# Kernel optimization log

Measured on AMD Instinct MI355X. Metric: run time of the kernel, lower is better.

Reference implementation:

```python
import jax, jax.numpy as jnp
import numpy as np

EPS = 1e-8

def _gelu(x):
    return jax.nn.gelu(x, approximate=False)  # torch F.gelu default (erf)

def _film_pool(feat, q, film_w, film_b, hid_w, hid_b, fin_w, fin_b):
    # feat: (B,C,H,W), q: (B,Q,E)
    B, C, H, W = feat.shape
    f = feat.reshape(B, C, H * W).transpose(0, 2, 1)            # (B,HW,C)
    gb = q @ film_w + film_b                                    # (B,Q,2C)
    gamma, beta = jnp.split(gb, 2, axis=-1)                     # (B,Q,C) each
    mod = gamma[:, :, None, :] * f[:, None, :, :] + beta[:, :, None, :]  # (B,Q,HW,C)
    h = _gelu(mod @ hid_w + hid_b)                              # (B,Q,HW,Hh)
    attn = jax.nn.sigmoid(h @ fin_w + fin_b)                    # (B,Q,HW,1)
    pooled = (attn * mod).sum(axis=2) / (attn.sum(axis=2) + EPS)  # (B,Q,C)
    return pooled, attn[..., 0]                                 # attn map (B,Q,HW)

def setup_inputs() -> dict:
    key = jax.random.key(0)
    ks = jax.random.split(key, 32)
    B, Q, E, Hh = 2, 32, 768, 128
    chans = [64, 128, 256]
    hws = [(80, 80), (40, 40), (20, 20)]
    d = {}
    d['feat0'] = jax.random.normal(ks[0], (B, chans[0], *hws[0]), jnp.float32)
    d['feat1'] = jax.random.normal(ks[1], (B, chans[1], *hws[1]), jnp.float32)
    d['feat2'] = jax.random.normal(ks[2], (B, chans[2], *hws[2]), jnp.float32)
    d['fact_embeddings'] = jax.random.normal(ks[3], (B, Q, E), jnp.float32)
    for i, C in enumerate(chans):
        d[f'film_w{i}'] = jax.random.normal(ks[4 + 4 * i], (E, 2 * C), jnp.float32) * 0.02
        d[f'film_b{i}'] = jnp.zeros((2 * C,), jnp.float32)
        d[f'hid_w{i}'] = jax.random.normal(ks[5 + 4 * i], (C, Hh), jnp.float32) * 0.05
        d[f'hid_b{i}'] = jnp.zeros((Hh,), jnp.float32)
        d[f'fin_w{i}'] = jax.random.normal(ks[6 + 4 * i], (Hh, 1), jnp.float32) * 0.05
        d[f'fin_b{i}'] = jnp.zeros((1,), jnp.float32)
    in_dim = sum(chans) + hws[-1][0] * hws[-1][1]  # 448 + 400 = 848
    d['mlp_w1'] = jax.random.normal(ks[20], (in_dim, 512), jnp.float32) * 0.02
    d['mlp_b1'] = jnp.zeros((512,), jnp.float32)
    d['mlp_w2'] = jax.random.normal(ks[21], (512, 256), jnp.float32) * 0.02
    d['mlp_b2'] = jnp.zeros((256,), jnp.float32)
    d['mlp_w3'] = jax.random.normal(ks[22], (256, 1), jnp.float32) * 0.02
    d['mlp_b3'] = jnp.zeros((1,), jnp.float32)
    return d

def reference(feat0, feat1, feat2, fact_embeddings,
              film_w0, film_b0, hid_w0, hid_b0, fin_w0, fin_b0,
              film_w1, film_b1, hid_w1, hid_b1, fin_w1, fin_b1,
              film_w2, film_b2, hid_w2, hid_b2, fin_w2, fin_b2,
              mlp_w1, mlp_b1, mlp_w2, mlp_b2, mlp_w3, mlp_b3):
    q = fact_embeddings
    p0, _ = _film_pool(feat0, q, film_w0, film_b0, hid_w0, hid_b0, fin_w0, fin_b0)
    p1, _ = _film_pool(feat1, q, film_w1, film_b1, hid_w1, hid_b1, fin_w1, fin_b1)
    p2, a2 = _film_pool(feat2, q, film_w2, film_b2, hid_w2, hid_b2, fin_w2, fin_b2)
    cat = jnp.concatenate([p0, p1, p2, a2], axis=2)  # (B,Q,848)
    x = _gelu(cat @ mlp_w1 + mlp_b1)
    x = _gelu(x @ mlp_w2 + mlp_b2)
    logits = (x @ mlp_w3 + mlp_b3)[..., 0]  # (B,Q)
    return logits
```

## Files before the change

kernel.cpp:

```cpp
#include <hip/hip_runtime.h>
#include <math.h>

#define BQ 64
#define HH 128
#define EPS 1e-8f

typedef short bf16x8 __attribute__((ext_vector_type(8)));
typedef float f32x4  __attribute__((ext_vector_type(4)));

typedef const __attribute__((address_space(1))) void* gptr_t;
typedef __attribute__((address_space(3))) void* lptr_t;

__device__ __forceinline__ float gelu_exact(float x) {
    return 0.5f * x * (1.0f + erff(x * 0.70710678118654752440f));
}

__device__ __forceinline__ unsigned bf16_rne(float x) {
    unsigned u = __float_as_uint(x);
    return (u + 0x7FFFu + ((u >> 16) & 1u)) >> 16;
}
__device__ __forceinline__ uint2 split_pack(float a, float b) {
    unsigned ha = bf16_rne(a);
    float fa = __uint_as_float(ha << 16);
    unsigned la = bf16_rne(a - fa);
    unsigned hb = bf16_rne(b);
    float fb = __uint_as_float(hb << 16);
    unsigned lb = bf16_rne(b - fb);
    uint2 r; r.x = ha | (hb << 16); r.y = la | (lb << 16);
    return r;
}

__device__ __forceinline__
void pack_feat_body(int i,
                    const float* __restrict__ f0, const float* __restrict__ f1,
                    const float* __restrict__ f2,
                    unsigned short* __restrict__ p0h, unsigned short* __restrict__ p0l,
                    unsigned short* __restrict__ p1h, unsigned short* __restrict__ p1l,
                    unsigned short* __restrict__ p2h, unsigned short* __restrict__ p2l)
{
    const float* f; unsigned short *oh, *ol; int HW; int idx;
    if (i < 102400)      { f = f0; oh = p0h; ol = p0l; HW = 6400; idx = i; }
    else if (i < 153600) { f = f1; oh = p1h; ol = p1l; HW = 1600; idx = i - 102400; }
    else if (i < 179200) { f = f2; oh = p2h; ol = p2l; HW = 400;  idx = i - 153600; }
    else return;
    const int px = idx % HW;
    const int cgb = idx / HW;
    const float* src = f + ((size_t)cgb * 8) * HW + px;
    float a[8];
    #pragma unroll
    for (int k = 0; k < 8; ++k) a[k] = src[(size_t)k * HW];
    unsigned hwd[4], lwd[4];
    #pragma unroll
    for (int k = 0; k < 4; ++k) {
        uint2 p = split_pack(a[2 * k], a[2 * k + 1]);
        hwd[k] = p.x; lwd[k] = p.y;
    }
    *(uint4*)&oh[(size_t)idx * 8] = make_uint4(hwd[0], hwd[1], hwd[2], hwd[3]);
    *(uint4*)&ol[(size_t)idx * 8] = make_uint4(lwd[0], lwd[1], lwd[2], lwd[3]);
}

__global__ __launch_bounds__(256)
void prep1_kernel(const float* __restrict__ f0, const float* __restrict__ f1,
                  const float* __restrict__ f2,
                  unsigned short* __restrict__ p0h, unsigned short* __restrict__ p0l,
                  unsigned short* __restrict__ p1h, unsigned short* __restrict__ p1l,
                  unsigned short* __restrict__ p2h, unsigned short* __restrict__ p2l,
                  const float* __restrict__ qe,
                  const float* __restrict__ fw0, const float* __restrict__ fb0,
                  const float* __restrict__ fw1, const float* __restrict__ fb1,
                  const float* __restrict__ fw2, const float* __restrict__ fb2,
                  float* __restrict__ gb0, float* __restrict__ gb1, float* __restrict__ gb2)
{
    const int tid = threadIdx.x;
    if (blockIdx.x < 700) {
        pack_feat_body(blockIdx.x * 256 + tid, f0, f1, f2, p0h, p0l, p1h, p1l, p2h, p2l);
        return;
    }
    __shared__ float sq[768];
    __shared__ float sP[256];
    const int bb = blockIdx.x - 700;
    const int chunk = bb >> 6, bq = bb & 63;
    int s, o0;
    if (chunk == 0)      { s = 0; o0 = 0; }
    else if (chunk <= 2) { s = 1; o0 = (chunk - 1) * 128; }
    else                 { s = 2; o0 = (chunk - 3) * 128; }
    const float* fw  = s == 0 ? fw0 : s == 1 ? fw1 : fw2;
    const float* fbv = s == 0 ? fb0 : s == 1 ? fb1 : fb2;
    float* gb        = s == 0 ? gb0 : s == 1 ? gb1 : gb2;
    const int twoC = 128 << s;

    for (int i = tid; i < 768; i += 256) sq[i] = qe[bq * 768 + i];
    __syncthreads();
    const int o = o0 + (tid & 127), half = tid >> 7;
    const int e0 = half * 384;
    float a0 = 0.f, a1 = 0.f;
    #pragma unroll 2
    for (int e = 0; e < 384; e += 2) {
        a0 = fmaf(sq[e0 + e],     fw[(e0 + e) * twoC + o],     a0);
        a1 = fmaf(sq[e0 + e + 1], fw[(e0 + e + 1) * twoC + o], a1);
    }
    sP[tid] = a0 + a1;
    __syncthreads();
    if (tid < 128) {
        int oo = o0 + tid;
        gb[bq * twoC + oo] = sP[tid] + sP[tid + 128] + fbv[oo];
    }
}

__global__ __launch_bounds__(256)
void prep2_kernel(const float* __restrict__ gb0, const float* __restrict__ gb1,
                  const float* __restrict__ gb2,
                  const float* __restrict__ hw0_, const float* __restrict__ hb0,
                  const float* __restrict__ hw1_, const float* __restrict__ hb1,
                  const float* __restrict__ hw2_, const float* __restrict__ hb2,
                  unsigned short* __restrict__ g0h, unsigned short* __restrict__ g0l,
                  unsigned short* __restrict__ g1h, unsigned short* __restrict__ g1l,
                  unsigned short* __restrict__ g2h, unsigned short* __restrict__ g2l,
                  float* __restrict__ b20, float* __restrict__ b21, float* __restrict__ b22)
{
    const int tid = threadIdx.x;
    if (blockIdx.x < 1792) {
        int i = blockIdx.x * 256 + tid;
        const float *gb, *hw; unsigned short *oh, *ol; int C, idx;
        if (i < 65536)       { gb = gb0; hw = hw0_; oh = g0h; ol = g0l; C = 64;  idx = i; }
        else if (i < 196608) { gb = gb1; hw = hw1_; oh = g1h; ol = g1l; C = 128; idx = i - 65536; }
        else                 { gb = gb2; hw = hw2_; oh = g2h; ol = g2l; C = 256; idx = i - 196608; }
        const int j  = idx & 127;
        const int cg = (idx >> 7) % (C / 8);
        const int bq = idx / (128 * (C / 8));
        const int c0 = cg * 8;
        const float* g = gb + bq * 2 * C;
        float a[8];
        #pragma unroll
        for (int k = 0; k < 8; ++k) a[k] = g[c0 + k] * hw[(size_t)(c0 + k) * HH + j];
        unsigned hwd[4], lwd[4];
        #pragma unroll
        for (int k = 0; k < 4; ++k) {
            uint2 p = split_pack(a[2 * k], a[2 * k + 1]);
            hwd[k] = p.x; lwd[k] = p.y;
        }
        *(uint4*)&oh[(size_t)idx * 8] = make_uint4(hwd[0], hwd[1], hwd[2], hwd[3]);
        *(uint4*)&ol[(size_t)idx * 8] = make_uint4(lwd[0], lwd[1], lwd[2], lwd[3]);
        return;
    }
    __shared__ float sBeta[256];
    __shared__ float sP[256];
    const int bb = blockIdx.x - 1792;
    const int s = bb >> 6, bq = bb & 63;
    const float* gb = s == 0 ? gb0 : s == 1 ? gb1 : gb2;
    const float* hw = s == 0 ? hw0_ : s == 1 ? hw1_ : hw2_;
    const float* hb = s == 0 ? hb0 : s == 1 ? hb1 : hb2;
    float* b2       = s == 0 ? b20 : s == 1 ? b21 : b22;
    const int C = 64 << s;

    for (int i = tid; i < C; i += 256) sBeta[i] = gb[bq * 2 * C + C + i];
    __syncthreads();
    const int j = tid & 127, half = tid >> 7;
    const int c0 = half * (C / 2);
    float acc = 0.f;
    for (int c = 0; c < C / 2; ++c)
        acc = fmaf(sBeta[c0 + c], hw[(c0 + c) * HH + j], acc);
    sP[tid] = acc;
    __syncthreads();
    if (tid < 128) b2[bq * HH + tid] = hb[tid] + sP[tid] + sP[tid + 128];
}

#define MFMA3(ACC, ALO, AHI, BH, BL)                                            \
    ACC = __builtin_amdgcn_mfma_f32_16x16x32_bf16(ALO, BH, ACC, 0, 0, 0);       \
    ACC = __builtin_amdgcn_mfma_f32_16x16x32_bf16(AHI, BL, ACC, 0, 0, 0);       \
    ACC = __builtin_amdgcn_mfma_f32_16x16x32_bf16(AHI, BH, ACC, 0, 0, 0);

template<int C, bool WRITE_ATTN>
__device__ __forceinline__
void pool_body(const float* __restrict__ feat, int HW,
               const unsigned short* __restrict__ fh, const unsigned short* __restrict__ fl,
               const unsigned short* __restrict__ gwh, const unsigned short* __restrict__ gwl,
               const float* __restrict__ b2, const float* __restrict__ finw,
               const float* __restrict__ finb,
               float* __restrict__ Sout, float* __restrict__ attn_out,
               int b, int qp, int tile,
               unsigned short* sB, float* sAttn)
{
    const int tid  = threadIdx.x;
    const int w    = tid >> 6;
    const int lane = tid & 63;
    const int l15  = lane & 15, l4 = lane >> 4;
    const int px0  = tile * 256;
    constexpr int CG  = C / 8;
    constexpr int NKS = CG / 4;
    const int bq0 = b * 32 + qp * 2;
    const int bq1 = bq0 + 1;
    const float* fbase = feat + (size_t)b * C * HW;

    f32x4 accA[2][8], accB[2][8];
    #pragma unroll
    for (int jt = 0; jt < 8; ++jt) {
        float bv0 = b2[bq0 * HH + jt * 16 + l15];
        float bv1 = b2[bq1 * HH + jt * 16 + l15];
        accA[0][jt] = (f32x4){bv0, bv0, bv0, bv0};
        accA[1][jt] = (f32x4){bv0, bv0, bv0, bv0};
        accB[0][jt] = (f32x4){bv1, bv1, bv1, bv1};
        accB[1][jt] = (f32x4){bv1, bv1, bv1, bv1};
    }

    const int apx0 = min(px0 + (w * 2 + 0) * 16 + l15, HW - 1);
    const int apx1 = min(px0 + (w * 2 + 1) * 16 + l15, HW - 1);
    const unsigned short* fhp = fh + (size_t)b * CG * HW * 8;
    const unsigned short* flp = fl + (size_t)b * CG * HW * 8;
    const unsigned short* qsrc0 = gwh + (size_t)bq0 * CG * 1024;
    const unsigned short* qsrc1 = gwl + (size_t)bq0 * CG * 1024;
    const unsigned short* qsrc2 = gwh + (size_t)bq1 * CG * 1024;
    const unsigned short* qsrc3 = gwl + (size_t)bq1 * CG * 1024;

    const int lane8 = lane * 8;
    const int woff  = __builtin_amdgcn_readfirstlane(w * 512);

    #define STAGE(KS, BUF)                                                       \
    {                                                                            \
        const unsigned short* s0 = qsrc0 + (size_t)(KS) * 4096 + woff + lane8;   \
        const unsigned short* s1 = qsrc1 + (size_t)(KS) * 4096 + woff + lane8;   \
        const unsigned short* s2 = qsrc2 + (size_t)(KS) * 4096 + woff + lane8;   \
        const unsigned short* s3 = qsrc3 + (size_t)(KS) * 4096 + woff + lane8;   \
        __builtin_amdgcn_global_load_lds((gptr_t)s0, (lptr_t)((BUF) + 0    + woff), 16, 0, 0); \
        __builtin_amdgcn_global_load_lds((gptr_t)s1, (lptr_t)((BUF) + 4096 + woff), 16, 0, 0); \
        __builtin_amdgcn_global_load_lds((gptr_t)s2, (lptr_t)((BUF) + 8192 + woff), 16, 0, 0); \
        __builtin_amdgcn_global_load_lds((gptr_t)s3, (lptr_t)((BUF) + 12288 + woff), 16, 0, 0); \
    }

    STAGE(0, sB)

    for (int ks = 0; ks < NKS; ++ks) {
        __syncthreads();
        unsigned short* cur = sB + (ks & 1) * 16384;
        if (ks + 1 < NKS) STAGE(ks + 1, sB + (((ks + 1) & 1) * 16384))

        const size_t arow = (size_t)(ks * 4 + l4) * HW;
        const bf16x8 Ahi0 = *(const bf16x8*)(fhp + (arow + apx0) * 8);
        const bf16x8 Alo0 = *(const bf16x8*)(flp + (arow + apx0) * 8);
        const bf16x8 Ahi1 = *(const bf16x8*)(fhp + (arow + apx1) * 8);
        const bf16x8 Alo1 = *(const bf16x8*)(flp + (arow + apx1) * 8);

        const int bofs = (l4 * 128 + l15) * 8;
        #pragma unroll
        for (int jt = 0; jt < 8; ++jt) {
            const bf16x8 B0h = *(const bf16x8*)(cur + bofs + jt * 128);
            const bf16x8 B0l = *(const bf16x8*)(cur + 4096 + bofs + jt * 128);
            MFMA3(accA[0][jt], Alo0, Ahi0, B0h, B0l)
            MFMA3(accA[1][jt], Alo1, Ahi1, B0h, B0l)
            const bf16x8 B1h = *(const bf16x8*)(cur + 8192 + bofs + jt * 128);
            const bf16x8 B1l = *(const bf16x8*)(cur + 12288 + bofs + jt * 128);
            MFMA3(accB[0][jt], Alo0, Ahi0, B1h, B1l)
            MFMA3(accB[1][jt], Alo1, Ahi1, B1h, B1l)
        }
    }
    #undef STAGE

    const float fb0 = finb[0];
    #pragma unroll
    for (int pt = 0; pt < 2; ++pt) {
        float p0[4] = {0.f, 0.f, 0.f, 0.f};
        float p1[4] = {0.f, 0.f, 0.f, 0.f};
        #pragma unroll
        for (int jt = 0; jt < 8; ++jt) {
            float fwv = finw[jt * 16 + l15];
            #pragma unroll
            for (int r = 0; r < 4; ++r) {
                p0[r] = fmaf(gelu_exact(accA[pt][jt][r]), fwv, p0[r]);
                p1[r] = fmaf(gelu_exact(accB[pt][jt][r]), fwv, p1[r]);
            }
        }
        #pragma unroll
        for (int r = 0; r < 4; ++r) {
            p0[r] += __shfl_xor(p0[r], 1);  p1[r] += __shfl_xor(p1[r], 1);
            p0[r] += __shfl_xor(p0[r], 2);  p1[r] += __shfl_xor(p1[r], 2);
            p0[r] += __shfl_xor(p0[r], 4);  p1[r] += __shfl_xor(p1[r], 4);
            p0[r] += __shfl_xor(p0[r], 8);  p1[r] += __shfl_xor(p1[r], 8);
        }
        if (l15 == 0) {
            #pragma unroll
            for (int r = 0; r < 4; ++r) {
                int lpx = (w * 2 + pt) * 16 + l4 * 4 + r;
                int px  = px0 + lpx;
                float a0v = (px < HW) ? 1.0f / (1.0f + expf(-(p0[r] + fb0))) : 0.0f;
                float a1v = (px < HW) ? 1.0f / (1.0f + expf(-(p1[r] + fb0))) : 0.0f;
                sAttn[lpx]       = a0v;
                sAttn[256 + lpx] = a1v;
                if (WRITE_ATTN && px < HW) {
                    attn_out[bq0 * HW + px] = a0v;
                    attn_out[bq1 * HW + px] = a1v;
                }
            }
        }
    }
    __syncthreads();

    {
        float sa = sAttn[tid];
        #pragma unroll
        for (int d = 1; d < 64; d <<= 1) sa += __shfl_xor(sa, d);
        if (lane == 0) {
            int bqx = (tid < 256) ? bq0 : bq1;
            atomicAdd(&Sout[bqx * (C + 1) + C], sa);
        }
    }

    constexpr int CPW = C / 8;
    #pragma unroll 1
    for (int ci = 0; ci < CPW; ++ci) {
        const int c2 = w * CPW + ci;
        const float* fr = fbase + (size_t)c2 * HW;
        float s0 = 0.f, s1 = 0.f;
        #pragma unroll
        for (int k = 0; k < 4; ++k) {
            int lpx = lane + 64 * k;
            int gc = min(px0 + lpx, HW - 1);
            float fv = fr[gc];
            s0 = fmaf(fv, sAttn[lpx], s0);
            s1 = fmaf(fv, sAttn[256 + lpx], s1);
        }
        #pragma unroll
        for (int d = 1; d < 64; d <<= 1) {
            s0 += __shfl_xor(s0, d);
            s1 += __shfl_xor(s1, d);
        }
        if (lane == 0) {
            atomicAdd(&Sout[bq0 * (C + 1) + c2], s0);
            atomicAdd(&Sout[bq1 * (C + 1) + c2], s1);
        }
    }
}

__global__ __launch_bounds__(512)
void pool_fused(const unsigned short* __restrict__ f0h, const unsigned short* __restrict__ f0l,
                const unsigned short* __restrict__ f1h, const unsigned short* __restrict__ f1l,
                const unsigned short* __restrict__ f2h, const unsigned short* __restrict__ f2l,
                const unsigned short* __restrict__ g0h, const unsigned short* __restrict__ g0l,
                const unsigned short* __restrict__ g1h, const unsigned short* __restrict__ g1l,
                const unsigned short* __restrict__ g2h, const unsigned short* __restrict__ g2l,
                const float* __restrict__ feat0, const float* __restrict__ feat1,
                const float* __restrict__ feat2,
                const float* __restrict__ b20, const float* __restrict__ b21,
                const float* __restrict__ b22,
                const float* __restrict__ finw0, const float* __restrict__ finb0,
                const float* __restrict__ finw1, const float* __restrict__ finb1,
                const float* __restrict__ finw2, const float* __restrict__ finb2,
                float* __restrict__ S0, float* __restrict__ S1, float* __restrict__ S2,
                float* __restrict__ attn2)
{
    __shared__ __align__(16) unsigned short sB[32768];
    float* sAttn = (float*)sB;

    const int blk0 = blockIdx.x;
    const int xcd = blk0 & 7, s = blk0 >> 3;
    int k, t;
    if (s < 8)       { k = s >> 1;            t = s & 1; }
    else if (s < 36) { k = 4 + (s - 8) / 7;   t = (s - 8) % 7; }
    else             { k = 8 + (s - 36) / 25; t = (s - 36) % 25; }
    const int b  = xcd >> 2;
    const int qp = (k & 3) * 4 + (xcd & 3);
    const int sidx = k >> 2;

    if (sidx == 0) {
        pool_body<256, true>(feat2, 400, f2h, f2l, g2h, g2l, b22, finw2, finb2,
                             S2, attn2, b, qp, t, sB, sAttn);
    } else if (sidx == 1) {
        pool_body<128, false>(feat1, 1600, f1h, f1l, g1h, g1l, b21, finw1, finb1,
                              S1, nullptr, b, qp, t, sB, sAttn);
    } else {
        pool_body<64, false>(feat0, 6400, f0h, f0l, g0h, g0l, b20, finw0, finb0,
                             S0, nullptr, b, qp, t, sB, sAttn);
    }
}

__global__ __launch_bounds__(256)
void mlp1_kernel(const float* __restrict__ S0, const float* __restrict__ S1,
                 const float* __restrict__ S2,
                 const float* __restrict__ gb0, const float* __restrict__ gb1,
                 const float* __restrict__ gb2,
                 const float* __restrict__ attn2,
                 const float* __restrict__ w1, const float* __restrict__ b1,
                 float* __restrict__ X1)
{
    __shared__ float sCat[848];
    __shared__ float sP[256];
    const int tid = threadIdx.x, bq = blockIdx.x;

    for (int i = tid; i < 448; i += 256) {
        int sc, c;
        if (i < 64)       { sc = 0; c = i; }
        else if (i < 192) { sc = 1; c = i - 64; }
        else              { sc = 2; c = i - 192; }
        const int C = 64 << sc;
        const float* So = (sc == 0) ? S0 : (sc == 1) ? S1 : S2;
        const float* g  = (sc == 0) ? gb0 : (sc == 1) ? gb1 : gb2;
        float Sa = So[bq * (C + 1) + C];
        float Sf = So[bq * (C + 1) + c];
        float gamma = g[bq * 2 * C + c];
        float beta  = g[bq * 2 * C + C + c];
        sCat[i] = (gamma * Sf + beta * Sa) / (Sa + EPS);
    }
    for (int i = tid; i < 400; i += 256) sCat[448 + i] = attn2[bq * 400 + i];
    __syncthreads();

    const int o = blockIdx.y * 128 + (tid & 127), half = tid >> 7;
    const int k0 = half * 424;
    float a0 = 0.f, a1 = 0.f;
    #pragma unroll 2
    for (int k = 0; k < 424; k += 2) {
        a0 = fmaf(sCat[k0 + k],     w1[(k0 + k) * 512 + o],     a0);
        a1 = fmaf(sCat[k0 + k + 1], w1[(k0 + k + 1) * 512 + o], a1);
    }
    sP[tid] = a0 + a1;
    __syncthreads();
    if (tid < 128) {
        int oo = blockIdx.y * 128 + tid;
        X1[bq * 512 + oo] = sP[tid] + sP[tid + 128] + b1[oo];
    }
}

__global__ __launch_bounds__(256)
void mlp23_kernel(const float* __restrict__ X1,
                  const float* __restrict__ w2, const float* __restrict__ b2,
                  const float* __restrict__ w3, const float* __restrict__ b3,
                  float* __restrict__ out)
{
    __shared__ float sX1[512];
    __shared__ float sX2[256];
    __shared__ float sR[4];
    const int tid = threadIdx.x, bq = blockIdx.x;
    for (int i = tid; i < 512; i += 256) sX1[i] = gelu_exact(X1[bq * 512 + i]);
    __syncthreads();
    float a0 = b2[tid], a1 = 0.f, a2 = 0.f, a3 = 0.f;
    #pragma unroll 4
    for (int k = 0; k < 512; k += 4) {
        a0 = fmaf(sX1[k],     w2[(k)     * 256 + tid], a0);
        a1 = fmaf(sX1[k + 1], w2[(k + 1) * 256 + tid], a1);
        a2 = fmaf(sX1[k + 2], w2[(k + 2) * 256 + tid], a2);
        a3 = fmaf(sX1[k + 3], w2[(k + 3) * 256 + tid], a3);
    }
    sX2[tid] = gelu_exact((a0 + a1) + (a2 + a3));
    __syncthreads();
    float p = sX2[tid] * w3[tid];
    #pragma unroll
    for (int d = 1; d < 64; d <<= 1) p += __shfl_xor(p, d);
    if ((tid & 63) == 0) sR[tid >> 6] = p;
    __syncthreads();
    if (tid == 0) out[bq] = sR[0] + sR[1] + sR[2] + sR[3] + b3[0];
}

extern "C" void kernel_launch(void* const* d_in, const int* in_sizes, int n_in,
                              void* d_out, int out_size, void* d_ws, size_t ws_size,
                              hipStream_t stream)
{
    const float* feat0 = (const float*)d_in[0];
    const float* feat1 = (const float*)d_in[1];
    const float* feat2 = (const float*)d_in[2];
    const float* qe    = (const float*)d_in[3];
    const float* film_w0 = (const float*)d_in[4];
    const float* film_b0 = (const float*)d_in[5];
    const float* hid_w0  = (const float*)d_in[6];
    const float* hid_b0  = (const float*)d_in[7];
    const float* fin_w0  = (const float*)d_in[8];
    const float* fin_b0  = (const float*)d_in[9];
    const float* film_w1 = (const float*)d_in[10];
    const float* film_b1 = (const float*)d_in[11];
    const float* hid_w1  = (const float*)d_in[12];
    const float* hid_b1  = (const float*)d_in[13];
    const float* fin_w1  = (const float*)d_in[14];
    const float* fin_b1  = (const float*)d_in[15];
    const float* film_w2 = (const float*)d_in[16];
    const float* film_b2 = (const float*)d_in[17];
    const float* hid_w2  = (const float*)d_in[18];
    const float* hid_b2  = (const float*)d_in[19];
    const float* fin_w2  = (const float*)d_in[20];
    const float* fin_b2  = (const float*)d_in[21];
    const float* mlp_w1  = (const float*)d_in[22];
    const float* mlp_b1  = (const float*)d_in[23];
    const float* mlp_w2  = (const float*)d_in[24];
    const float* mlp_b2  = (const float*)d_in[25];
    const float* mlp_w3  = (const float*)d_in[26];
    const float* mlp_b3  = (const float*)d_in[27];

    float* ws = (float*)d_ws;
    float* S0    = ws;
    float* S1    = ws + 4160;
    float* S2    = ws + 12416;
    float* gb0   = ws + 28864;
    float* gb1   = ws + 37056;
    float* gb2   = ws + 53440;
    float* b20   = ws + 86208;
    float* b21   = ws + 94400;
    float* b22   = ws + 102592;
    float* attn2 = ws + 110784;
    float* X1    = ws + 136384;

    unsigned short* us = (unsigned short*)(ws + 169216);
    unsigned short* f0h = us;
    unsigned short* f0l = f0h + 819200;
    unsigned short* f1h = f0l + 819200;
    unsigned short* f1l = f1h + 409600;
    unsigned short* f2h = f1l + 409600;
    unsigned short* f2l = f2h + 204800;
    unsigned short* g0h = f2l + 204800;
    unsigned short* g0l = g0h + 524288;
    unsigned short* g1h = g0l + 524288;
    unsigned short* g1l = g1h + 1048576;
    unsigned short* g2h = g1l + 1048576;
    unsigned short* g2l = g2h + 2097152;

    hipMemsetAsync(d_ws, 0, 28864 * sizeof(float), stream);

    prep1_kernel<<<1148, 256, 0, stream>>>(
        feat0, feat1, feat2, f0h, f0l, f1h, f1l, f2h, f2l,
        qe, film_w0, film_b0, film_w1, film_b1, film_w2, film_b2,
        gb0, gb1, gb2);

    prep2_kernel<<<1984, 256, 0, stream>>>(
        gb0, gb1, gb2,
        hid_w0, hid_b0, hid_w1, hid_b1, hid_w2, hid_b2,
        g0h, g0l, g1h, g1l, g2h, g2l,
        b20, b21, b22);

    pool_fused<<<1088, 512, 0, stream>>>(
        f0h, f0l, f1h, f1l, f2h, f2l,
        g0h, g0l, g1h, g1l, g2h, g2l,
        feat0, feat1, feat2,
        b20, b21, b22,
        fin_w0, fin_b0, fin_w1, fin_b1, fin_w2, fin_b2,
        S0, S1, S2, attn2);

    mlp1_kernel<<<dim3(BQ, 4), 256, 0, stream>>>(
        S0, S1, S2, gb0, gb1, gb2, attn2, mlp_w1, mlp_b1, X1);

    mlp23_kernel<<<BQ, 256, 0, stream>>>(
        X1, mlp_w2, mlp_b2, mlp_w3, mlp_b3, (float*)d_out);
}
```

Baseline: 246.7 us.

## Fold memset into prep, pipeline A loads, reorder pool blocks, fuse MLP kernels

The workspace memset moves into extra blocks of prep1, which removes a separate launch. The pool main loop is unrolled by two so the A-fragment global loads for the next K-step are issued before the current MFMAs. The pooled-feature reduction reads the split-bf16 packed features instead of the original fp32 maps, and the block index mapping drops its XCD-aware ordering in favour of a simple linear one. The two MLP kernels become one 512-thread kernel per query, which removes a launch and the X1 round trip, but runs the first layer on only 64 blocks.

After: 268.2 us. +8.7%, slower.

```diff
diff --git a/kernel.cpp b/kernel.cpp
--- a/kernel.cpp
+++ b/kernel.cpp
@@ -28,6 +28,9 @@
     unsigned lb = bf16_rne(b - fb);
     uint2 r; r.x = ha | (hb << 16); r.y = la | (lb << 16);
     return r;
+}
+__device__ __forceinline__ float bf_to_f(unsigned short u) {
+    return __uint_as_float((unsigned)u << 16);
 }
 
 __device__ __forceinline__
@@ -69,11 +72,17 @@
                   const float* __restrict__ fw0, const float* __restrict__ fb0,
                   const float* __restrict__ fw1, const float* __restrict__ fb1,
                   const float* __restrict__ fw2, const float* __restrict__ fb2,
-                  float* __restrict__ gb0, float* __restrict__ gb1, float* __restrict__ gb2)
+                  float* __restrict__ gb0, float* __restrict__ gb1, float* __restrict__ gb2,
+                  float* __restrict__ zws)
 {
     const int tid = threadIdx.x;
     if (blockIdx.x < 700) {
         pack_feat_body(blockIdx.x * 256 + tid, f0, f1, f2, p0h, p0l, p1h, p1l, p2h, p2l);
+        return;
+    }
+    if (blockIdx.x >= 1148) {
+        int idx = (blockIdx.x - 1148) * 256 + tid;
+        if (idx < 28864) zws[idx] = 0.0f;
         return;
     }
     __shared__ float sq[768];
@@ -172,7 +181,7 @@
 
 template<int C, bool WRITE_ATTN>
 __device__ __forceinline__
-void pool_body(const float* __restrict__ feat, int HW,
+void pool_body(int HW,
                const unsigned short* __restrict__ fh, const unsigned short* __restrict__ fl,
                const unsigned short* __restrict__ gwh, const unsigned short* __restrict__ gwl,
                const float* __restrict__ b2, const float* __restrict__ finw,
@@ -190,7 +199,6 @@
     constexpr int NKS = CG / 4;
     const int bq0 = b * 32 + qp * 2;
     const int bq1 = bq0 + 1;
-    const float* fbase = feat + (size_t)b * C * HW;
 
     f32x4 accA[2][8], accB[2][8];
     #pragma unroll
@@ -221,39 +229,57 @@
         const unsigned short* s1 = qsrc1 + (size_t)(KS) * 4096 + woff + lane8;   \
         const unsigned short* s2 = qsrc2 + (size_t)(KS) * 4096 + woff + lane8;   \
         const unsigned short* s3 = qsrc3 + (size_t)(KS) * 4096 + woff + lane8;   \
-        __builtin_amdgcn_global_load_lds((gptr_t)s0, (lptr_t)((BUF) + 0    + woff), 16, 0, 0); \
-        __builtin_amdgcn_global_load_lds((gptr_t)s1, (lptr_t)((BUF) + 4096 + woff), 16, 0, 0); \
-        __builtin_amdgcn_global_load_lds((gptr_t)s2, (lptr_t)((BUF) + 8192 + woff), 16, 0, 0); \
+        __builtin_amdgcn_global_load_lds((gptr_t)s0, (lptr_t)((BUF) + 0     + woff), 16, 0, 0); \
+        __builtin_amdgcn_global_load_lds((gptr_t)s1, (lptr_t)((BUF) + 4096  + woff), 16, 0, 0); \
+        __builtin_amdgcn_global_load_lds((gptr_t)s2, (lptr_t)((BUF) + 8192  + woff), 16, 0, 0); \
         __builtin_amdgcn_global_load_lds((gptr_t)s3, (lptr_t)((BUF) + 12288 + woff), 16, 0, 0); \
     }
 
+    #define LOADA(KS, H0, L0, H1, L1)                                            \
+    {                                                                            \
+        const size_t ar = (size_t)((KS) * 4 + l4) * HW;                          \
+        H0 = *(const bf16x8*)(fhp + (ar + apx0) * 8);                            \
+        L0 = *(const bf16x8*)(flp + (ar + apx0) * 8);                            \
+        H1 = *(const bf16x8*)(fhp + (ar + apx1) * 8);                            \
+        L1 = *(const bf16x8*)(flp + (ar + apx1) * 8);                            \
+    }
+
+    #define MFMAB(CUR, H0, L0, H1, L1)                                           \
+    {                                                                            \
+        const int bofs = (l4 * 128 + l15) * 8;                                   \
+        _Pragma("unroll")                                                        \
+        for (int jt = 0; jt < 8; ++jt) {                                         \
+            const bf16x8 B0h = *(const bf16x8*)((CUR) + bofs + jt * 128);        \
+            const bf16x8 B0l = *(const bf16x8*)((CUR) + 4096 + bofs + jt * 128); \
+            MFMA3(accA[0][jt], L0, H0, B0h, B0l)                                 \
+            MFMA3(accA[1][jt], L1, H1, B0h, B0l)                                 \
+            const bf16x8 B1h = *(const bf16x8*)((CUR) + 8192 + bofs + jt * 128); \
+            const bf16x8 B1l = *(const bf16x8*)((CUR) + 12288 + bofs + jt * 128);\
+            MFMA3(accB[0][jt], L0, H0, B1h, B1l)                                 \
+            MFMA3(accB[1][jt], L1, H1, B1h, B1l)                                 \
+        }                                                                        \
+    }
+
+    bf16x8 cA0h, cA0l, cA1h, cA1l, nA0h, nA0l, nA1h, nA1l;
     STAGE(0, sB)
-
-    for (int ks = 0; ks < NKS; ++ks) {
+    LOADA(0, cA0h, cA0l, cA1h, cA1l)
+
+    #pragma unroll 1
+    for (int ks = 0; ks < NKS; ks += 2) {
         __syncthreads();
-        unsigned short* cur = sB + (ks & 1) * 16384;
-        if (ks + 1 < NKS) STAGE(ks + 1, sB + (((ks + 1) & 1) * 16384))
-
-        const size_t arow = (size_t)(ks * 4 + l4) * HW;
-        const bf16x8 Ahi0 = *(const bf16x8*)(fhp + (arow + apx0) * 8);
-        const bf16x8 Alo0 = *(const bf16x8*)(flp + (arow + apx0) * 8);
-        const bf16x8 Ahi1 = *(const bf16x8*)(fhp + (arow + apx1) * 8);
-        const bf16x8 Alo1 = *(const bf16x8*)(flp + (arow + apx1) * 8);
-
-        const int bofs = (l4 * 128 + l15) * 8;
-        #pragma unroll
-        for (int jt = 0; jt < 8; ++jt) {
-            const bf16x8 B0h = *(const bf16x8*)(cur + bofs + jt * 128);
-            const bf16x8 B0l = *(const bf16x8*)(cur + 4096 + bofs + jt * 128);
-            MFMA3(accA[0][jt], Alo0, Ahi0, B0h, B0l)
-            MFMA3(accA[1][jt], Alo1, Ahi1, B0h, B0l)
-            const bf16x8 B1h = *(const bf16x8*)(cur + 8192 + bofs + jt * 128);
-            const bf16x8 B1l = *(const bf16x8*)(cur + 12288 + bofs + jt * 128);
-            MFMA3(accB[0][jt], Alo0, Ahi0, B1h, B1l)
-            MFMA3(accB[1][jt], Alo1, Ahi1, B1h, B1l)
-        }
+        LOADA(ks + 1, nA0h, nA0l, nA1h, nA1l)
+        STAGE(ks + 1, sB + 16384)
+        MFMAB(sB, cA0h, cA0l, cA1h, cA1l)
+        __syncthreads();
+        if (ks + 2 < NKS) {
+            LOADA(ks + 2, cA0h, cA0l, cA1h, cA1l)
+            STAGE(ks + 2, sB)
+        }
+        MFMAB(sB + 16384, nA0h, nA0l, nA1h, nA1l)
     }
     #undef STAGE
+    #undef LOADA
+    #undef MFMAB
 
     const float fb0 = finb[0];
     #pragma unroll
@@ -308,13 +334,14 @@
     #pragma unroll 1
     for (int ci = 0; ci < CPW; ++ci) {
         const int c2 = w * CPW + ci;
-        const float* fr = fbase + (size_t)c2 * HW;
+        const unsigned short* ph = fhp + ((size_t)(c2 >> 3) * HW) * 8 + (c2 & 7);
+        const unsigned short* pl = flp + ((size_t)(c2 >> 3) * HW) * 8 + (c2 & 7);
         float s0 = 0.f, s1 = 0.f;
         #pragma unroll
         for (int k = 0; k < 4; ++k) {
             int lpx = lane + 64 * k;
             int gc = min(px0 + lpx, HW - 1);
-            float fv = fr[gc];
+            float fv = bf_to_f(ph[(size_t)gc * 8]) + bf_to_f(pl[(size_t)gc * 8]);
             s0 = fmaf(fv, sAttn[lpx], s0);
             s1 = fmaf(fv, sAttn[256 + lpx], s1);
         }
@@ -337,8 +364,6 @@
                 const unsigned short* __restrict__ g0h, const unsigned short* __restrict__ g0l,
                 const unsigned short* __restrict__ g1h, const unsigned short* __restrict__ g1l,
                 const unsigned short* __restrict__ g2h, const unsigned short* __restrict__ g2l,
-                const float* __restrict__ feat0, const float* __restrict__ feat1,
-                const float* __restrict__ feat2,
                 const float* __restrict__ b20, const float* __restrict__ b21,
                 const float* __restrict__ b22,
                 const float* __restrict__ finw0, const float* __restrict__ finb0,
@@ -350,46 +375,48 @@
     __shared__ __align__(16) unsigned short sB[32768];
     float* sAttn = (float*)sB;
 
-    const int blk0 = blockIdx.x;
-    const int xcd = blk0 & 7, s = blk0 >> 3;
-    int k, t;
-    if (s < 8)       { k = s >> 1;            t = s & 1; }
-    else if (s < 36) { k = 4 + (s - 8) / 7;   t = (s - 8) % 7; }
-    else             { k = 8 + (s - 36) / 25; t = (s - 36) % 25; }
-    const int b  = xcd >> 2;
-    const int qp = (k & 3) * 4 + (xcd & 3);
-    const int sidx = k >> 2;
-
-    if (sidx == 0) {
-        pool_body<256, true>(feat2, 400, f2h, f2l, g2h, g2l, b22, finw2, finb2,
+    const int blk = blockIdx.x;
+    if (blk < 64) {
+        int bt = blk >> 4, qp = blk & 15;
+        int b = bt >> 1, t = bt & 1;
+        pool_body<256, true>(400, f2h, f2l, g2h, g2l, b22, finw2, finb2,
                              S2, attn2, b, qp, t, sB, sAttn);
-    } else if (sidx == 1) {
-        pool_body<128, false>(feat1, 1600, f1h, f1l, g1h, g1l, b21, finw1, finb1,
+    } else if (blk < 288) {
+        int bb = blk - 64; int bt = bb >> 4, qp = bb & 15;
+        int b = bt / 7, t = bt % 7;
+        pool_body<128, false>(1600, f1h, f1l, g1h, g1l, b21, finw1, finb1,
                               S1, nullptr, b, qp, t, sB, sAttn);
     } else {
-        pool_body<64, false>(feat0, 6400, f0h, f0l, g0h, g0l, b20, finw0, finb0,
+        int bb = blk - 288; int bt = bb >> 4, qp = bb & 15;
+        int b = bt / 25, t = bt % 25;
+        pool_body<64, false>(6400, f0h, f0l, g0h, g0l, b20, finw0, finb0,
                              S0, nullptr, b, qp, t, sB, sAttn);
     }
 }
 
-__global__ __launch_bounds__(256)
-void mlp1_kernel(const float* __restrict__ S0, const float* __restrict__ S1,
-                 const float* __restrict__ S2,
-                 const float* __restrict__ gb0, const float* __restrict__ gb1,
-                 const float* __restrict__ gb2,
-                 const float* __restrict__ attn2,
-                 const float* __restrict__ w1, const float* __restrict__ b1,
-                 float* __restrict__ X1)
+__global__ __launch_bounds__(512)
+void mlp_fused(const float* __restrict__ S0, const float* __restrict__ S1,
+               const float* __restrict__ S2,
+               const float* __restrict__ gb0, const float* __restrict__ gb1,
+               const float* __restrict__ gb2,
+               const float* __restrict__ attn2,
+               const float* __restrict__ w1, const float* __restrict__ b1,
+               const float* __restrict__ w2, const float* __restrict__ mb2,
+               const float* __restrict__ w3, const float* __restrict__ b3,
+               float* __restrict__ out)
 {
     __shared__ float sCat[848];
-    __shared__ float sP[256];
+    __shared__ float sX1[512];
+    __shared__ float sP[512];
+    __shared__ float sX2[256];
+    __shared__ float sR[4];
     const int tid = threadIdx.x, bq = blockIdx.x;
 
-    for (int i = tid; i < 448; i += 256) {
+    if (tid < 448) {
         int sc, c;
-        if (i < 64)       { sc = 0; c = i; }
-        else if (i < 192) { sc = 1; c = i - 64; }
-        else              { sc = 2; c = i - 192; }
+        if (tid < 64)       { sc = 0; c = tid; }
+        else if (tid < 192) { sc = 1; c = tid - 64; }
+        else                { sc = 2; c = tid - 192; }
         const int C = 64 << sc;
         const float* So = (sc == 0) ? S0 : (sc == 1) ? S1 : S2;
         const float* g  = (sc == 0) ? gb0 : (sc == 1) ? gb1 : gb2;
@@ -397,53 +424,43 @@
         float Sf = So[bq * (C + 1) + c];
         float gamma = g[bq * 2 * C + c];
         float beta  = g[bq * 2 * C + C + c];
-        sCat[i] = (gamma * Sf + beta * Sa) / (Sa + EPS);
-    }
-    for (int i = tid; i < 400; i += 256) sCat[448 + i] = attn2[bq * 400 + i];
-    __syncthreads();
-
-    const int o = blockIdx.y * 128 + (tid & 127), half = tid >> 7;
-    const int k0 = half * 424;
-    float a0 = 0.f, a1 = 0.f;
-    #pragma unroll 2
-    for (int k = 0; k < 424; k += 2) {
-        a0 = fmaf(sCat[k0 + k],     w1[(k0 + k) * 512 + o],     a0);
-        a1 = fmaf(sCat[k0 + k + 1], w1[(k0 + k + 1) * 512 + o], a1);
-    }
-    sP[tid] = a0 + a1;
-    __syncthreads();
-    if (tid < 128) {
-        int oo = blockIdx.y * 128 + tid;
-        X1[bq * 512 + oo] = sP[tid] + sP[tid + 128] + b1[oo];
-    }
-}
-
-__global__ __launch_bounds__(256)
-void mlp23_kernel(const float* __restrict__ X1,
-                  const float* __restrict__ w2, const float* __restrict__ b2,
-                  const float* __restrict__ w3, const float* __restrict__ b3,
-                  float* __restrict__ out)
-{
-    __shared__ float sX1[512];
-    __shared__ float sX2[256];
-    __shared__ float sR[4];
-    const int tid = threadIdx.x, bq = blockIdx.x;
-    for (int i = tid; i < 512; i += 256) sX1[i] = gelu_exact(X1[bq * 512 + i]);
-    __syncthreads();
-    float a0 = b2[tid], a1 = 0.f, a2 = 0.f, a3 = 0.f;
-    #pragma unroll 4
-    for (int k = 0; k < 512; k += 4) {
-        a0 = fmaf(sX1[k],     w2[(k)     * 256 + tid], a0);
-        a1 = fmaf(sX1[k + 1], w2[(k + 1) * 256 + tid], a1);
-        a2 = fmaf(sX1[k + 2], w2[(k + 2) * 256 + tid], a2);
-        a3 = fmaf(sX1[k + 3], w2[(k + 3) * 256 + tid], a3);
-    }
-    sX2[tid] = gelu_exact((a0 + a1) + (a2 + a3));
-    __syncthreads();
-    float p = sX2[tid] * w3[tid];
-    #pragma unroll
-    for (int d = 1; d < 64; d <<= 1) p += __shfl_xor(p, d);
-    if ((tid & 63) == 0) sR[tid >> 6] = p;
+        sCat[tid] = (gamma * Sf + beta * Sa) / (Sa + EPS);
+    }
+    if (tid < 400) sCat[448 + tid] = attn2[bq * 400 + tid];
+    __syncthreads();
+
+    {
+        float a0 = 0.f, a1 = 0.f;
+        #pragma unroll 2
+        for (int k = 0; k < 848; k += 2) {
+            a0 = fmaf(sCat[k],     w1[(size_t)k * 512 + tid],       a0);
+            a1 = fmaf(sCat[k + 1], w1[(size_t)(k + 1) * 512 + tid], a1);
+        }
+        sX1[tid] = gelu_exact(a0 + a1 + b1[tid]);
+    }
+    __syncthreads();
+
+    {
+        const int o = tid & 255, half = tid >> 8;
+        const int k0 = half * 256;
+        float a0 = 0.f, a1 = 0.f;
+        #pragma unroll 2
+        for (int k = 0; k < 256; k += 2) {
+            a0 = fmaf(sX1[k0 + k],     w2[(size_t)(k0 + k) * 256 + o],     a0);
+            a1 = fmaf(sX1[k0 + k + 1], w2[(size_t)(k0 + k + 1) * 256 + o], a1);
+        }
+        sP[tid] = a0 + a1;
+    }
+    __syncthreads();
+    if (tid < 256) sX2[tid] = gelu_exact(sP[tid] + sP[tid + 256] + mb2[tid]);
+    __syncthreads();
+
+    if (tid < 256) {
+        float p = sX2[tid] * w3[tid];
+        #pragma unroll
+        for (int d = 1; d < 64; d <<= 1) p += __shfl_xor(p, d);
+        if ((tid & 63) == 0) sR[tid >> 6] = p;
+    }
     __syncthreads();
     if (tid == 0) out[bq] = sR[0] + sR[1] + sR[2] + sR[3] + b3[0];
 }
@@ -492,7 +509,6 @@
     float* b21   = ws + 94400;
     float* b22   = ws + 102592;
     float* attn2 = ws + 110784;
-    float* X1    = ws + 136384;
 
     unsigned short* us = (unsigned short*)(ws + 169216);
     unsigned short* f0h = us;
@@ -508,12 +524,10 @@
     unsigned short* g2h = g1l + 1048576;
     unsigned short* g2l = g2h + 2097152;
 
-    hipMemsetAsync(d_ws, 0, 28864 * sizeof(float), stream);
-
-    prep1_kernel<<<1148, 256, 0, stream>>>(
+    prep1_kernel<<<1261, 256, 0, stream>>>(
         feat0, feat1, feat2, f0h, f0l, f1h, f1l, f2h, f2l,
         qe, film_w0, film_b0, film_w1, film_b1, film_w2, film_b2,
-        gb0, gb1, gb2);
+        gb0, gb1, gb2, ws);
 
     prep2_kernel<<<1984, 256, 0, stream>>>(
         gb0, gb1, gb2,
@@ -524,14 +538,12 @@
     pool_fused<<<1088, 512, 0, stream>>>(
         f0h, f0l, f1h, f1l, f2h, f2l,
         g0h, g0l, g1h, g1l, g2h, g2l,
-        feat0, feat1, feat2,
         b20, b21, b22,
         fin_w0, fin_b0, fin_w1, fin_b1, fin_w2, fin_b2,
         S0, S1, S2, attn2);
 
-    mlp1_kernel<<<dim3(BQ, 4), 256, 0, stream>>>(
-        S0, S1, S2, gb0, gb1, gb2, attn2, mlp_w1, mlp_b1, X1);
-
-    mlp23_kernel<<<BQ, 256, 0, stream>>>(
-        X1, mlp_w2, mlp_b2, mlp_w3, mlp_b3, (float*)d_out);
-}
+    mlp_fused<<<BQ, 512, 0, stream>>>(
+        S0, S1, S2, gb0, gb1, gb2, attn2,
+        mlp_w1, mlp_b1, mlp_w2, mlp_b2, mlp_w3, mlp_b3,
+        (float*)d_out);
+}
```
